# Kernel optimization log

Measured on AMD Instinct MI355X. Metric: run time of the kernel, lower is better.

Reference implementation:

```python
import jax, jax.numpy as jnp
import numpy as np

B, D = 4096, 1024

def setup_inputs() -> dict:
    key = jax.random.key(0)
    k1, k2, k3 = jax.random.split(key, 3)
    # q, p are row-stochastic probability distributions (original calls q.log())
    q = jax.nn.softmax(jax.random.normal(k1, (B, D), dtype=jnp.float32), axis=-1)
    p = jax.nn.softmax(jax.random.normal(k2, (B, D), dtype=jnp.float32), axis=-1)
    # binary same-class indicator matrix
    labels_matrix = jax.random.randint(k3, (B, B), 0, 2).astype(jnp.float32)
    return {"q": q, "p": p, "labels_matrix": labels_matrix}

def reference(q, p, labels_matrix):
    d = q.shape[1]
    log_q = jnp.log(q)
    log_p = jnp.log(p)
    # torch kl_div(log_q, p) = p * (log p - log q); mean over feature dim -> [B]
    kl_div = jnp.mean(p * (log_p - log_q), axis=1)
    # pairwise kl_dis[i, j] = mean_d p[j,d] * (log p[j,d] - log q[i,d])
    # = (sum_d p[j] log p[j] - (log_q @ p^T)[i, j]) / D  -- single GEMM, no BxBxD tensor
    p_entropy_term = jnp.sum(p * log_p, axis=1)          # [B]
    cross = log_q @ p.T                                   # [B, B]
    kl_dis = (p_entropy_term[None, :] - cross) / d        # [B, B]
    # original detaches kl_dis via .cpu().numpy()
    kl_dis = jax.lax.stop_gradient(kl_dis)
    positive = kl_div + jnp.sum(kl_dis * labels_matrix, axis=1)
    negative = jnp.sum(kl_dis * (1.0 - labels_matrix), axis=1)
    return jnp.sum(positive / negative)
```

## Files before the change

kernel.cpp:

```cpp
#include <hip/hip_runtime.h>
#include <hip/hip_bf16.h>
#include <stdint.h>

#define BROWS 4096
#define DDIM  1024

typedef __bf16 bf16_t;
typedef __bf16 bf16x8 __attribute__((ext_vector_type(8)));
typedef float  f32x4  __attribute__((ext_vector_type(4)));

#define LDS_STRIDE 68

__device__ __forceinline__ unsigned short f2bf_bits(float f) {
    union { float f; unsigned int u; } v; v.f = f;
    unsigned int u = v.u;
    unsigned int r = (u + 0x7fffu + ((u >> 16) & 1u)) >> 16;
    return (unsigned short)r;
}

__global__ __launch_bounds__(256) void prep_kernel(
    const float* __restrict__ q, const float* __restrict__ p,
    const float* __restrict__ L,
    bf16_t* __restrict__ lqb, bf16_t* __restrict__ pb,
    uint64_t* __restrict__ Lb,
    float* __restrict__ e, float* __restrict__ kld,
    float* __restrict__ CS, float* __restrict__ CL, float* __restrict__ EL)
{
    const int row = blockIdx.x;
    const int t   = threadIdx.x;
    const int wv  = t >> 6, ln = t & 63;

    const float4* q4 = (const float4*)(q + (size_t)row * DDIM);
    const float4* p4 = (const float4*)(p + (size_t)row * DDIM);
    float4 qv = q4[t];
    float4 pv = p4[t];

    float lq0 = __logf(qv.x), lq1 = __logf(qv.y), lq2 = __logf(qv.z), lq3 = __logf(qv.w);
    float lp0 = __logf(pv.x), lp1 = __logf(pv.y), lp2 = __logf(pv.z), lp3 = __logf(pv.w);

    float esum = pv.x * lp0 + pv.y * lp1 + pv.z * lp2 + pv.w * lp3;
    float ksum = pv.x * (lp0 - lq0) + pv.y * (lp1 - lq1)
               + pv.z * (lp2 - lq2) + pv.w * (lp3 - lq3);

    ushort4 uq, up;
    uq.x = f2bf_bits(lq0); uq.y = f2bf_bits(lq1); uq.z = f2bf_bits(lq2); uq.w = f2bf_bits(lq3);
    up.x = f2bf_bits(pv.x); up.y = f2bf_bits(pv.y); up.z = f2bf_bits(pv.z); up.w = f2bf_bits(pv.w);
    ((ushort4*)(lqb + (size_t)row * DDIM))[t] = uq;
    ((ushort4*)(pb  + (size_t)row * DDIM))[t] = up;

    const float* Lrow = L + (size_t)row * BROWS;
    #pragma unroll
    for (int c = 0; c < 16; c++) {
        float v = Lrow[c * 256 + t];
        unsigned long long m = __ballot(v != 0.0f);
        if (ln == 0) Lb[(size_t)row * 64 + c * 4 + wv] = m;
    }

    if (t == 0) { CS[row] = 0.f; CL[row] = 0.f; EL[row] = 0.f; }

    #pragma unroll
    for (int off = 32; off > 0; off >>= 1) {
        esum += __shfl_down(esum, off);
        ksum += __shfl_down(ksum, off);
    }
    __shared__ float se[4], sk[4];
    if (ln == 0) { se[wv] = esum; sk[wv] = ksum; }
    __syncthreads();
    if (t == 0) {
        e[row]   = se[0] + se[1] + se[2] + se[3];
        kld[row] = (sk[0] + sk[1] + sk[2] + sk[3]) * (1.0f / DDIM);
    }
}

__global__ __launch_bounds__(512, 4) void gemm_epi_kernel(
    const bf16_t* __restrict__ Abf,
    const bf16_t* __restrict__ Bbf,
    const uint64_t* __restrict__ Lb,
    const float*  __restrict__ e,
    float* __restrict__ CS, float* __restrict__ CL, float* __restrict__ EL)
{
    __shared__ __align__(16) bf16_t As[256 * LDS_STRIDE];
    __shared__ __align__(16) bf16_t Bs[128 * LDS_STRIDE];

    const int t    = threadIdx.x;
    const int i0   = blockIdx.y * 256;
    const int j0   = blockIdx.x * 128;
    const int wave = t >> 6;
    const int lane = t & 63;
    const int q4   = lane >> 4;
    const int ln   = lane & 15;
    const int wrow = wave & 3;
    const int wcol = wave >> 2;

    f32x4 acc[4][4];
    #pragma unroll
    for (int a = 0; a < 4; a++)
        #pragma unroll
        for (int b = 0; b < 4; b++)
            acc[a][b] = (f32x4){0.f, 0.f, 0.f, 0.f};

    const bf16_t* gAp[4]; int lA[4];
    const bf16_t* gBp[2]; int lB[2];
    #pragma unroll
    for (int n = 0; n < 4; n++) {
        const int id = t + n * 512;
        gAp[n] = Abf + (size_t)(i0 + (id >> 3)) * DDIM + (id & 7) * 8;
        lA[n]  = (id >> 3) * LDS_STRIDE + (id & 7) * 8;
    }
    #pragma unroll
    for (int n = 0; n < 2; n++) {
        const int id = t + n * 512;
        gBp[n] = Bbf + (size_t)(j0 + (id >> 3)) * DDIM + (id & 7) * 8;
        lB[n]  = (id >> 3) * LDS_STRIDE + (id & 7) * 8;
    }

    bf16x8 pfA[4], pfB[2];
    #pragma unroll
    for (int n = 0; n < 4; n++) pfA[n] = *(const bf16x8*)(gAp[n]);
    #pragma unroll
    for (int n = 0; n < 2; n++) pfB[n] = *(const bf16x8*)(gBp[n]);

    #pragma unroll 1
    for (int c = 0; c < DDIM / 64; ++c) {
        __syncthreads();
        #pragma unroll
        for (int n = 0; n < 4; n++) *(bf16x8*)(As + lA[n]) = pfA[n];
        #pragma unroll
        for (int n = 0; n < 2; n++) *(bf16x8*)(Bs + lB[n]) = pfB[n];
        __syncthreads();

        if (c < DDIM / 64 - 1) {
            const int k = (c + 1) * 64;
            #pragma unroll
            for (int n = 0; n < 4; n++) pfA[n] = *(const bf16x8*)(gAp[n] + k);
            #pragma unroll
            for (int n = 0; n < 2; n++) pfB[n] = *(const bf16x8*)(gBp[n] + k);
        }

        #pragma unroll
        for (int ks = 0; ks < 2; ks++) {
            bf16x8 af[4], bfr[4];
            #pragma unroll
            for (int mi = 0; mi < 4; mi++)
                af[mi] = *(const bf16x8*)(As + (wrow * 64 + mi * 16 + ln) * LDS_STRIDE
                                             + ks * 32 + q4 * 8);
            #pragma unroll
            for (int ni = 0; ni < 4; ni++)
                bfr[ni] = *(const bf16x8*)(Bs + (wcol * 64 + ni * 16 + ln) * LDS_STRIDE
                                              + ks * 32 + q4 * 8);
            #pragma unroll
            for (int mi = 0; mi < 4; mi++)
                #pragma unroll
                for (int ni = 0; ni < 4; ni++)
                    acc[mi][ni] = __builtin_amdgcn_mfma_f32_16x16x32_bf16(
                        af[mi], bfr[ni], acc[mi][ni], 0, 0, 0);
        }
    }

    const int i_base = i0 + wrow * 64;
    const int j_base = j0 + wcol * 64;

    float e_j[4];
    #pragma unroll
    for (int ni = 0; ni < 4; ni++) e_j[ni] = e[j_base + ni * 16 + ln];

    #pragma unroll
    for (int mi = 0; mi < 4; mi++) {
        #pragma unroll
        for (int r = 0; r < 4; r++) {
            const int i = i_base + mi * 16 + q4 * 4 + r;
            const uint64_t m  = Lb[(size_t)i * 64 + (j_base >> 6)];
            const uint64_t ms = m >> ln;
            float cs = 0.f, cl = 0.f, el = 0.f;
            #pragma unroll
            for (int ni = 0; ni < 4; ni++) {
                float c = acc[mi][ni][r];
                cs += c;
                if ((ms >> (ni * 16)) & 1ull) { cl += c; el += e_j[ni]; }
            }
            #pragma unroll
            for (int s = 1; s < 16; s <<= 1) {
                cs += __shfl_xor(cs, s);
                cl += __shfl_xor(cl, s);
                el += __shfl_xor(el, s);
            }
            if (ln == 0) {
                atomicAdd(&CS[i], cs);
                atomicAdd(&CL[i], cl);
                atomicAdd(&EL[i], el);
            }
        }
    }
}

__global__ __launch_bounds__(256) void final_kernel(
    const float* __restrict__ e, const float* __restrict__ kld,
    const float* __restrict__ CS, const float* __restrict__ CL,
    const float* __restrict__ EL, float* __restrict__ out)
{
    __shared__ float sred[4];
    __shared__ float sEtot;
    const int t = threadIdx.x;

    float s = 0.f;
    for (int j = t; j < BROWS; j += 256) s += e[j];
    #pragma unroll
    for (int off = 32; off > 0; off >>= 1) s += __shfl_down(s, off);
    if ((t & 63) == 0) sred[t >> 6] = s;
    __syncthreads();
    if (t == 0) sEtot = sred[0] + sred[1] + sred[2] + sred[3];
    __syncthreads();
    const float Etot = sEtot;
    const float invD = 1.0f / DDIM;

    float rs = 0.f;
    for (int i = t; i < BROWS; i += 256) {
        float el = EL[i], cl = CL[i], cs = CS[i];
        float pos = kld[i] + (el - cl) * invD;
        float neg = (Etot - el - cs + cl) * invD;
        rs += pos / neg;
    }
    __syncthreads();
    #pragma unroll
    for (int off = 32; off > 0; off >>= 1) rs += __shfl_down(rs, off);
    if ((t & 63) == 0) sred[t >> 6] = rs;
    __syncthreads();
    if (t == 0) out[0] = sred[0] + sred[1] + sred[2] + sred[3];
}

extern "C" void kernel_launch(void* const* d_in, const int* in_sizes, int n_in,
                              void* d_out, int out_size, void* d_ws, size_t ws_size,
                              hipStream_t stream)
{
    const float* q = (const float*)d_in[0];
    const float* p = (const float*)d_in[1];
    const float* L = (const float*)d_in[2];
    float* out = (float*)d_out;

    char* ws = (char*)d_ws;
    bf16_t* lqb = (bf16_t*)ws;
    bf16_t* pb  = (bf16_t*)(ws + (size_t)BROWS * DDIM * 2);
    float*  e   = (float*)(ws + (size_t)BROWS * DDIM * 4);
    float*  kld = e + BROWS;
    float*  CS  = kld + BROWS;
    float*  CL  = CS + BROWS;
    float*  EL  = CL + BROWS;
    uint64_t* Lb = (uint64_t*)(EL + BROWS);

    prep_kernel<<<BROWS, 256, 0, stream>>>(q, p, L, lqb, pb, Lb, e, kld, CS, CL, EL);

    dim3 grid(BROWS / 128, BROWS / 256);
    gemm_epi_kernel<<<grid, 512, 0, stream>>>(lqb, pb, Lb, e, CS, CL, EL);

    final_kernel<<<1, 256, 0, stream>>>(e, kld, CS, CL, EL, out);
}
```

Before: 190.4 us.

## Switch cross GEMM to FP8 operands with 256x256 tiles and register double-buffering

The prep kernel now quantizes log q and a scaled p (times 64) to FP8 e4m3 instead of bf16. The GEMM uses fp8 MFMA, undoes the scale in the epilogue, and grows the block tile to 256x256 with 1024 threads, prefetching two K-chunks ahead in registers. This halves operand bytes and global/LDS traffic and improves tile reuse. The cost is much coarser precision on log q, which may hurt accuracy, plus possible dynamic register-array indexing. The final reduction kernel also moves to 1024 threads.

```diff
diff --git a/kernel.cpp b/kernel.cpp
--- a/kernel.cpp
+++ b/kernel.cpp
@@ -4,24 +4,22 @@
 
 #define BROWS 4096
 #define DDIM  1024
-
-typedef __bf16 bf16_t;
-typedef __bf16 bf16x8 __attribute__((ext_vector_type(8)));
-typedef float  f32x4  __attribute__((ext_vector_type(4)));
-
-#define LDS_STRIDE 68
-
-__device__ __forceinline__ unsigned short f2bf_bits(float f) {
-    union { float f; unsigned int u; } v; v.f = f;
-    unsigned int u = v.u;
-    unsigned int r = (u + 0x7fffu + ((u >> 16) & 1u)) >> 16;
-    return (unsigned short)r;
+#define LSTR  72
+
+typedef float f32x4 __attribute__((ext_vector_type(4)));
+#define PSCALE 64.0f
+#define INV_PSCALE 0.015625f
+
+__device__ __forceinline__ int pack4_fp8(float a, float b, float c, float d) {
+    int w = __builtin_amdgcn_cvt_pk_fp8_f32(a, b, 0, false);
+    w = __builtin_amdgcn_cvt_pk_fp8_f32(c, d, w, true);
+    return w;
 }
 
 __global__ __launch_bounds__(256) void prep_kernel(
     const float* __restrict__ q, const float* __restrict__ p,
     const float* __restrict__ L,
-    bf16_t* __restrict__ lqb, bf16_t* __restrict__ pb,
+    int* __restrict__ lq8, int* __restrict__ p8,
     uint64_t* __restrict__ Lb,
     float* __restrict__ e, float* __restrict__ kld,
     float* __restrict__ CS, float* __restrict__ CL, float* __restrict__ EL)
@@ -30,10 +28,10 @@
     const int t   = threadIdx.x;
     const int wv  = t >> 6, ln = t & 63;
 
-    const float4* q4 = (const float4*)(q + (size_t)row * DDIM);
-    const float4* p4 = (const float4*)(p + (size_t)row * DDIM);
-    float4 qv = q4[t];
-    float4 pv = p4[t];
+    const float4* qv4 = (const float4*)(q + (size_t)row * DDIM);
+    const float4* pv4 = (const float4*)(p + (size_t)row * DDIM);
+    float4 qv = qv4[t];
+    float4 pv = pv4[t];
 
     float lq0 = __logf(qv.x), lq1 = __logf(qv.y), lq2 = __logf(qv.z), lq3 = __logf(qv.w);
     float lp0 = __logf(pv.x), lp1 = __logf(pv.y), lp2 = __logf(pv.z), lp3 = __logf(pv.w);
@@ -42,11 +40,9 @@
     float ksum = pv.x * (lp0 - lq0) + pv.y * (lp1 - lq1)
                + pv.z * (lp2 - lq2) + pv.w * (lp3 - lq3);
 
-    ushort4 uq, up;
-    uq.x = f2bf_bits(lq0); uq.y = f2bf_bits(lq1); uq.z = f2bf_bits(lq2); uq.w = f2bf_bits(lq3);
-    up.x = f2bf_bits(pv.x); up.y = f2bf_bits(pv.y); up.z = f2bf_bits(pv.z); up.w = f2bf_bits(pv.w);
-    ((ushort4*)(lqb + (size_t)row * DDIM))[t] = uq;
-    ((ushort4*)(pb  + (size_t)row * DDIM))[t] = up;
+    lq8[row * 256 + t] = pack4_fp8(lq0, lq1, lq2, lq3);
+    p8 [row * 256 + t] = pack4_fp8(pv.x * PSCALE, pv.y * PSCALE,
+                                   pv.z * PSCALE, pv.w * PSCALE);
 
     const float* Lrow = L + (size_t)row * BROWS;
     #pragma unroll
@@ -72,19 +68,19 @@
     }
 }
 
-__global__ __launch_bounds__(512, 4) void gemm_epi_kernel(
-    const bf16_t* __restrict__ Abf,
-    const bf16_t* __restrict__ Bbf,
+__global__ __launch_bounds__(1024, 4) void gemm_epi_kernel(
+    const uint8_t* __restrict__ A8,
+    const uint8_t* __restrict__ B8,
     const uint64_t* __restrict__ Lb,
     const float*  __restrict__ e,
     float* __restrict__ CS, float* __restrict__ CL, float* __restrict__ EL)
 {
-    __shared__ __align__(16) bf16_t As[256 * LDS_STRIDE];
-    __shared__ __align__(16) bf16_t Bs[128 * LDS_STRIDE];
+    __shared__ __align__(16) uint8_t As[256 * LSTR];
+    __shared__ __align__(16) uint8_t Bs[256 * LSTR];
 
     const int t    = threadIdx.x;
     const int i0   = blockIdx.y * 256;
-    const int j0   = blockIdx.x * 128;
+    const int j0   = blockIdx.x * 256;
     const int wave = t >> 6;
     const int lane = t & 63;
     const int q4   = lane >> 4;
@@ -99,61 +95,46 @@
         for (int b = 0; b < 4; b++)
             acc[a][b] = (f32x4){0.f, 0.f, 0.f, 0.f};
 
-    const bf16_t* gAp[4]; int lA[4];
-    const bf16_t* gBp[2]; int lB[2];
-    #pragma unroll
-    for (int n = 0; n < 4; n++) {
-        const int id = t + n * 512;
-        gAp[n] = Abf + (size_t)(i0 + (id >> 3)) * DDIM + (id & 7) * 8;
-        lA[n]  = (id >> 3) * LDS_STRIDE + (id & 7) * 8;
-    }
-    #pragma unroll
-    for (int n = 0; n < 2; n++) {
-        const int id = t + n * 512;
-        gBp[n] = Bbf + (size_t)(j0 + (id >> 3)) * DDIM + (id & 7) * 8;
-        lB[n]  = (id >> 3) * LDS_STRIDE + (id & 7) * 8;
-    }
-
-    bf16x8 pfA[4], pfB[2];
-    #pragma unroll
-    for (int n = 0; n < 4; n++) pfA[n] = *(const bf16x8*)(gAp[n]);
-    #pragma unroll
-    for (int n = 0; n < 2; n++) pfB[n] = *(const bf16x8*)(gBp[n]);
+    const int srow = t >> 2;
+    const int scol = (t & 3) * 16;
+    const uint8_t* gA = A8 + (size_t)(i0 + srow) * DDIM + scol;
+    const uint8_t* gB = B8 + (size_t)(j0 + srow) * DDIM + scol;
+    const int loff = srow * LSTR + scol;
+
+    int4 pfA[2], pfB[2];
+    pfA[0] = *(const int4*)(gA);       pfB[0] = *(const int4*)(gB);
+    pfA[1] = *(const int4*)(gA + 64);  pfB[1] = *(const int4*)(gB + 64);
 
     #pragma unroll 1
     for (int c = 0; c < DDIM / 64; ++c) {
+        const int buf = c & 1;
         __syncthreads();
-        #pragma unroll
-        for (int n = 0; n < 4; n++) *(bf16x8*)(As + lA[n]) = pfA[n];
-        #pragma unroll
-        for (int n = 0; n < 2; n++) *(bf16x8*)(Bs + lB[n]) = pfB[n];
+        *(int4*)(As + loff) = pfA[buf];
+        *(int4*)(Bs + loff) = pfB[buf];
         __syncthreads();
 
-        if (c < DDIM / 64 - 1) {
-            const int k = (c + 1) * 64;
-            #pragma unroll
-            for (int n = 0; n < 4; n++) pfA[n] = *(const bf16x8*)(gAp[n] + k);
-            #pragma unroll
-            for (int n = 0; n < 2; n++) pfB[n] = *(const bf16x8*)(gBp[n] + k);
+        if (c + 2 < DDIM / 64) {
+            pfA[buf] = *(const int4*)(gA + (c + 2) * 64);
+            pfB[buf] = *(const int4*)(gB + (c + 2) * 64);
         }
 
         #pragma unroll
         for (int ks = 0; ks < 2; ks++) {
-            bf16x8 af[4], bfr[4];
+            long af[4], bfv[4];
             #pragma unroll
             for (int mi = 0; mi < 4; mi++)
-                af[mi] = *(const bf16x8*)(As + (wrow * 64 + mi * 16 + ln) * LDS_STRIDE
-                                             + ks * 32 + q4 * 8);
+                af[mi] = *(const long*)(As + (wrow * 64 + mi * 16 + ln) * LSTR
+                                           + ks * 32 + q4 * 8);
             #pragma unroll
             for (int ni = 0; ni < 4; ni++)
-                bfr[ni] = *(const bf16x8*)(Bs + (wcol * 64 + ni * 16 + ln) * LDS_STRIDE
-                                              + ks * 32 + q4 * 8);
+                bfv[ni] = *(const long*)(Bs + (wcol * 64 + ni * 16 + ln) * LSTR
+                                            + ks * 32 + q4 * 8);
             #pragma unroll
             for (int mi = 0; mi < 4; mi++)
                 #pragma unroll
                 for (int ni = 0; ni < 4; ni++)
-                    acc[mi][ni] = __builtin_amdgcn_mfma_f32_16x16x32_bf16(
-                        af[mi], bfr[ni], acc[mi][ni], 0, 0, 0);
+                    acc[mi][ni] = __builtin_amdgcn_mfma_f32_16x16x32_fp8_fp8(
+                        af[mi], bfv[ni], acc[mi][ni], 0, 0, 0);
         }
     }
 
@@ -185,36 +166,42 @@
                 el += __shfl_xor(el, s);
             }
             if (ln == 0) {
-                atomicAdd(&CS[i], cs);
-                atomicAdd(&CL[i], cl);
+                atomicAdd(&CS[i], cs * INV_PSCALE);
+                atomicAdd(&CL[i], cl * INV_PSCALE);
                 atomicAdd(&EL[i], el);
             }
         }
     }
 }
 
-__global__ __launch_bounds__(256) void final_kernel(
+__global__ __launch_bounds__(1024) void final_kernel(
     const float* __restrict__ e, const float* __restrict__ kld,
     const float* __restrict__ CS, const float* __restrict__ CL,
     const float* __restrict__ EL, float* __restrict__ out)
 {
-    __shared__ float sred[4];
+    __shared__ float sred[16];
     __shared__ float sEtot;
     const int t = threadIdx.x;
+    const int wv = t >> 6, ln = t & 63;
 
     float s = 0.f;
-    for (int j = t; j < BROWS; j += 256) s += e[j];
+    for (int j = t; j < BROWS; j += 1024) s += e[j];
     #pragma unroll
     for (int off = 32; off > 0; off >>= 1) s += __shfl_down(s, off);
-    if ((t & 63) == 0) sred[t >> 6] = s;
-    __syncthreads();
-    if (t == 0) sEtot = sred[0] + sred[1] + sred[2] + sred[3];
+    if (ln == 0) sred[wv] = s;
+    __syncthreads();
+    if (t == 0) {
+        float a = 0.f;
+        #pragma unroll
+        for (int k = 0; k < 16; k++) a += sred[k];
+        sEtot = a;
+    }
     __syncthreads();
     const float Etot = sEtot;
     const float invD = 1.0f / DDIM;
 
     float rs = 0.f;
-    for (int i = t; i < BROWS; i += 256) {
+    for (int i = t; i < BROWS; i += 1024) {
         float el = EL[i], cl = CL[i], cs = CS[i];
         float pos = kld[i] + (el - cl) * invD;
         float neg = (Etot - el - cs + cl) * invD;
@@ -223,9 +210,14 @@
     __syncthreads();
     #pragma unroll
     for (int off = 32; off > 0; off >>= 1) rs += __shfl_down(rs, off);
-    if ((t & 63) == 0) sred[t >> 6] = rs;
-    __syncthreads();
-    if (t == 0) out[0] = sred[0] + sred[1] + sred[2] + sred[3];
+    if (ln == 0) sred[wv] = rs;
+    __syncthreads();
+    if (t == 0) {
+        float a = 0.f;
+        #pragma unroll
+        for (int k = 0; k < 16; k++) a += sred[k];
+        out[0] = a;
+    }
 }
 
 extern "C" void kernel_launch(void* const* d_in, const int* in_sizes, int n_in,
@@ -238,19 +230,20 @@
     float* out = (float*)d_out;
 
     char* ws = (char*)d_ws;
-    bf16_t* lqb = (bf16_t*)ws;
-    bf16_t* pb  = (bf16_t*)(ws + (size_t)BROWS * DDIM * 2);
-    float*  e   = (float*)(ws + (size_t)BROWS * DDIM * 4);
-    float*  kld = e + BROWS;
-    float*  CS  = kld + BROWS;
-    float*  CL  = CS + BROWS;
-    float*  EL  = CL + BROWS;
+    int*  lq8 = (int*)ws;
+    int*  p8  = (int*)(ws + (size_t)BROWS * DDIM);
+    float* e  = (float*)(ws + (size_t)BROWS * DDIM * 2);
+    float* kld = e + BROWS;
+    float* CS  = kld + BROWS;
+    float* CL  = CS + BROWS;
+    float* EL  = CL + BROWS;
     uint64_t* Lb = (uint64_t*)(EL + BROWS);
 
-    prep_kernel<<<BROWS, 256, 0, stream>>>(q, p, L, lqb, pb, Lb, e, kld, CS, CL, EL);
-
-    dim3 grid(BROWS / 128, BROWS / 256);
-    gemm_epi_kernel<<<grid, 512, 0, stream>>>(lqb, pb, Lb, e, CS, CL, EL);
-
-    final_kernel<<<1, 256, 0, stream>>>(e, kld, CS, CL, EL, out);
-}
+    prep_kernel<<<BROWS, 256, 0, stream>>>(q, p, L, lq8, p8, Lb, e, kld, CS, CL, EL);
+
+    dim3 grid(BROWS / 256, BROWS / 256);
+    gemm_epi_kernel<<<grid, 1024, 0, stream>>>(
+        (const uint8_t*)lq8, (const uint8_t*)p8, Lb, e, CS, CL, EL);
+
+    final_kernel<<<1, 1024, 0, stream>>>(e, kld, CS, CL, EL, out);
+}
```

Result: slower. 203.5 us (+6.9%).
